# Kernel optimization log

Hardware: AMD Instinct MI355X
Metric: run time of the kernel (lower is better)

The kernel has to match this reference:

```python
import jax, jax.numpy as jnp
import numpy as np

B, C, RED, H, RANK = 32768, 1024, 4, 4, 16
CH = C // RED          # 256 hidden width after gated down-projection
DH = CH // H           # 64 head dim
RATIO = 0.5            # residual_ratio
LN_EPS = 1e-5


def setup_inputs() -> dict:
    key = jax.random.key(0)
    ks = iter(jax.random.split(key, 32))
    n = lambda shape, s=0.02: jax.random.normal(next(ks), shape, jnp.float32) * s
    return {
        "x": jax.random.normal(next(ks), (B, C), jnp.float32),
        # LayerNorm(c_in)
        "ln_g": jnp.ones((C,), jnp.float32),
        "ln_b": jnp.zeros((C,), jnp.float32),
        # gated linear: down_proj / gate_proj  (stored [in, out])
        "Wd": n((C, CH)), "bd": jnp.zeros((CH,), jnp.float32),
        "Wg": n((C, CH)), "bg": jnp.zeros((CH,), jnp.float32),
        # depthwise Conv1d(CH, CH, k=1, groups=CH) on length-1 seq -> per-channel affine
        "dw_w": n((CH,), 1.0), "dw_b": jnp.zeros((CH,), jnp.float32),
        # LightFNN: Linear-GELU-Linear
        "W1": n((CH, CH)), "b1": jnp.zeros((CH,), jnp.float32),
        "W2": n((CH, CH)), "b2": jnp.zeros((CH,), jnp.float32),
        # MHSA (seq_len = 1)
        "Wq": n((CH, CH)), "bq": jnp.zeros((CH,), jnp.float32),
        "Wk": n((CH, CH)), "bk": jnp.zeros((CH,), jnp.float32),
        "Wv": n((CH, CH)), "bv": jnp.zeros((CH,), jnp.float32),
        "Wo": n((CH, CH)), "bo": jnp.zeros((CH,), jnp.float32),
        # up_proj
        "Wu": n((CH, C)), "bu": jnp.zeros((C,), jnp.float32),
        # LoRA (bias-free)
        "Wld": n((C, RANK)), "Wlu": n((RANK, C)),
    }


def reference(x, ln_g, ln_b, Wd, bd, Wg, bg, dw_w, dw_b,
              W1, b1, W2, b2, Wq, bq, Wk, bk, Wv, bv, Wo, bo,
              Wu, bu, Wld, Wlu):
    residual = x
    # LayerNorm
    mu = jnp.mean(x, axis=-1, keepdims=True)
    var = jnp.mean(jnp.square(x - mu), axis=-1, keepdims=True)
    h = (x - mu) * jax.lax.rsqrt(var + LN_EPS) * ln_g + ln_b
    # gated linear unit
    h = (h @ Wd + bd) * jax.nn.sigmoid(h @ Wg + bg)          # [B, CH]
    # depthwise conv over length-1 sequence == per-channel affine
    h = h * dw_w + dw_b
    # light FFN
    h = jax.nn.gelu(h @ W1 + b1) @ W2 + b2
    # seq_len-1 self-attention: softmax over a single key is 1 => out = Wo(v)
    q = (h @ Wq + bq).reshape(B, H, DH)
    k = (h @ Wk + bk).reshape(B, H, DH)
    v = (h @ Wv + bv).reshape(B, H, DH)
    scores = jnp.sum(q * k, axis=-1, keepdims=True) / jnp.sqrt(jnp.float32(DH))  # [B,H,1]
    attn = jax.nn.softmax(scores, axis=-1)                   # == ones
    h = (attn * v).reshape(B, CH) @ Wo + bo
    # up projection + LoRA
    h = h @ Wu + bu                                          # [B, C]
    h = h + (h @ Wld) @ Wlu
    # dropout is identity at inference; weighted residual mix
    return RATIO * h + (1.0 - RATIO) * residual
```

## Files before the change

kernel.cpp:

```cpp
#include <hip/hip_runtime.h>
#include <hip/hip_bf16.h>
#include <stdint.h>


typedef float f32x4 __attribute__((ext_vector_type(4)));
typedef __bf16 bf16x8 __attribute__((ext_vector_type(8)));
typedef unsigned short u16x8 __attribute__((ext_vector_type(8)));
typedef unsigned short u16x4 __attribute__((ext_vector_type(4)));

#define LN_EPS 1e-5f

__device__ __forceinline__ unsigned short f2bf(float f) {
  unsigned int u = __float_as_uint(f);
  u += 0x7fffu + ((u >> 16) & 1u);
  return (unsigned short)(u >> 16);
}

__device__ __forceinline__ void bar_lds() {
  asm volatile("s_waitcnt lgkmcnt(0)\n\ts_barrier" ::: "memory");
}

__global__ __launch_bounds__(256) void k_prep(
    const float* __restrict__ ln_g, const float* __restrict__ ln_b,
    const float* __restrict__ Wd, const float* __restrict__ Wg,
    const float* __restrict__ dw_w, const float* __restrict__ dw_b,
    const float* __restrict__ W1, const float* __restrict__ b1,
    const float* __restrict__ W2, const float* __restrict__ b2,
    const float* __restrict__ Wv, const float* __restrict__ bv,
    const float* __restrict__ Wo, const float* __restrict__ bo,
    const float* __restrict__ Wu, const float* __restrict__ bu,
    const float* __restrict__ Wld, const float* __restrict__ Wlu,
    unsigned short* __restrict__ PGd, unsigned short* __restrict__ PGg,
    unsigned short* __restrict__ PW1, float* __restrict__ GP,
    float* __restrict__ b1p, float* __restrict__ X,
    float* __restrict__ Y, float* __restrict__ bcomb) {
  __shared__ alignas(16) char SMEM[32896];
  const int b = blockIdx.x, tid = threadIdx.x;

  if (b < 72) {
    float (*S)[257] = (float(*)[257])SMEM;
    const float* src; const float* scale; unsigned short* dst;
    int kc; int gpa = -1;
    if (b < 32)      { src = Wd; scale = ln_g; dst = PGd; kc = b;      gpa = 0; }
    else if (b < 64) { src = Wg; scale = ln_g; dst = PGg; kc = b - 32; gpa = 2; }
    else             { src = W1; scale = dw_w; dst = PW1; kc = b - 64; }
    float csg = 0.f, csb = 0.f;
    for (int r = 0; r < 32; ++r) {
      int k = kc * 32 + r;
      float raw = src[(size_t)k * 256 + tid];
      float v = scale[k] * raw;
      S[r][tid] = v;
      if (gpa >= 0) { csg += v; csb += ln_b[k] * raw; }
    }
    if (gpa >= 0) {
      GP[((size_t)gpa * 32 + kc) * 256 + tid] = csg;
      GP[((size_t)(gpa + 1) * 32 + kc) * 256 + tid] = csb;
    }
    __syncthreads();
    const int ntL = tid >> 4;
    #pragma unroll
    for (int c = 0; c < 4; ++c) {
      int lane = (tid * 4 + c) & 63;
      int kb = (lane >> 4) * 8, nl = ntL * 16 + (lane & 15);
      u16x8 o;
      #pragma unroll
      for (int j = 0; j < 8; ++j) o[j] = f2bf(S[kb + j][nl]);
      *(u16x8*)(dst + ((size_t)(kc * 16 + ntL) * 64 + lane) * 8) = o;
    }
  } else if (b == 72) {
    float s = 0.f;
    #pragma unroll 8
    for (int k = 0; k < 256; ++k) s += dw_b[k] * W1[k * 256 + tid];
    b1p[tid] = b1[tid] + s;
  } else if (b == 73) {
    float* F = (float*)SMEM;
    float* r1 = F;
    float* r2 = F + 256;
    float* r3 = F + 512;
    float* s16 = F + 1536;
    float* PART = F + 1552;
    float* sb = F + 1808;
    sb[tid] = b2[tid];
    __syncthreads();
    {
      float s = bv[tid];
      #pragma unroll 8
      for (int k = 0; k < 256; ++k) s += sb[k] * Wv[(size_t)k * 256 + tid];
      r1[tid] = s;
    }
    __syncthreads();
    {
      float s = bo[tid];
      #pragma unroll 8
      for (int k = 0; k < 256; ++k) s += r1[k] * Wo[(size_t)k * 256 + tid];
      r2[tid] = s;
    }
    __syncthreads();
    {
      float a0 = bu[tid], a1 = bu[tid + 256], a2 = bu[tid + 512], a3 = bu[tid + 768];
      #pragma unroll 4
      for (int k = 0; k < 256; ++k) {
        float rr = r2[k];
        const float* wr = Wu + (size_t)k * 1024 + tid;
        a0 += rr * wr[0]; a1 += rr * wr[256]; a2 += rr * wr[512]; a3 += rr * wr[768];
      }
      r3[tid] = a0; r3[tid + 256] = a1; r3[tid + 512] = a2; r3[tid + 768] = a3;
    }
    __syncthreads();
    {
      const int g = tid >> 4, s = tid & 15;
      float p = 0.f;
      #pragma unroll 4
      for (int n = g * 64; n < g * 64 + 64; ++n) p += r3[n] * Wld[(size_t)n * 16 + s];
      PART[g * 16 + s] = p;
    }
    __syncthreads();
    if (tid < 16) {
      float s = 0.f;
      #pragma unroll
      for (int g = 0; g < 16; ++g) s += PART[g * 16 + tid];
      s16[tid] = s;
    }
    __syncthreads();
    #pragma unroll
    for (int c = 0; c < 4; ++c) {
      int n = tid + c * 256;
      float v = r3[n];
      #pragma unroll
      for (int s = 0; s < 16; ++s) v += s16[s] * Wlu[(size_t)s * 1024 + n];
      bcomb[n] = v;
    }
  } else if (b < 90) {
    float (*SW)[257] = (float(*)[257])SMEM;
    const int r0 = (b - 74) * 16;
    #pragma unroll
    for (int r = 0; r < 16; ++r) SW[r][tid] = W2[(size_t)(r0 + r) * 256 + tid];
    __syncthreads();
    float acc[16];
    #pragma unroll
    for (int r = 0; r < 16; ++r) acc[r] = 0.f;
    #pragma unroll 4
    for (int n = 0; n < 256; ++n) {
      float wv = Wv[(size_t)n * 256 + tid];
      #pragma unroll
      for (int r = 0; r < 16; ++r) acc[r] += SW[r][n] * wv;
    }
    #pragma unroll
    for (int r = 0; r < 16; ++r) X[(size_t)(r0 + r) * 256 + tid] = acc[r];
  } else {
    float (*SW)[257] = (float(*)[257])SMEM;
    const int idx = b - 90, r0 = (idx >> 2) * 16, c0 = (idx & 3) * 256;
    #pragma unroll
    for (int r = 0; r < 16; ++r) SW[r][tid] = Wo[(size_t)(r0 + r) * 256 + tid];
    __syncthreads();
    float acc[16];
    #pragma unroll
    for (int r = 0; r < 16; ++r) acc[r] = 0.f;
    #pragma unroll 4
    for (int n = 0; n < 256; ++n) {
      float wu = Wu[(size_t)n * 1024 + c0 + tid];
      #pragma unroll
      for (int r = 0; r < 16; ++r) acc[r] += SW[r][n] * wu;
    }
    #pragma unroll
    for (int r = 0; r < 16; ++r) Y[(size_t)(r0 + r) * 1024 + c0 + tid] = acc[r];
  }
}

__global__ __launch_bounds__(256) void k_fold(
    const float* __restrict__ Y, const float* __restrict__ Wld,
    const float* __restrict__ Wlu, const float* __restrict__ GP,
    unsigned short* __restrict__ PY,
    float* __restrict__ gdvA, float* __restrict__ ggvA,
    float* __restrict__ bdA, float* __restrict__ bgA) {
  __shared__ alignas(16) char SMEM[32896];
  const int b = blockIdx.x, tid = threadIdx.x;
  if (b < 64) {
    float* F = (float*)SMEM;
    float* YLL = F;
    float* WL = F + 512;
    float* PART = F + 2560;
    unsigned short* TL = (unsigned short*)(SMEM + 10240);
    const int rb = b >> 3, ccol = (b & 7) * 128;
    {
      const int r = tid >> 3, g = tid & 7;
      const float* yrow = Y + (size_t)(rb * 32 + r) * 1024;
      float p[16];
      #pragma unroll
      for (int s = 0; s < 16; ++s) p[s] = 0.f;
      for (int n = g * 128; n < g * 128 + 128; ++n) {
        float yv = yrow[n];
        const float* wl = Wld + (size_t)n * 16;
        #pragma unroll
        for (int s = 0; s < 16; ++s) p[s] += yv * wl[s];
      }
      #pragma unroll
      for (int s = 0; s < 16; ++s) PART[(r * 16 + s) * 8 + g] = p[s];
    }
    __syncthreads();
    #pragma unroll
    for (int e2 = 0; e2 < 2; ++e2) {
      int e = tid + e2 * 256;
      float s = 0.f;
      #pragma unroll
      for (int g = 0; g < 8; ++g) s += PART[e * 8 + g];
      YLL[e] = s;
    }
    #pragma unroll
    for (int i = 0; i < 8; ++i) {
      int el = tid + i * 256;
      int s = el >> 7, n = el & 127;
      WL[el] = Wlu[(size_t)s * 1024 + ccol + n];
    }
    __syncthreads();
    const int r = tid >> 3, c0 = (tid & 7) * 16;
    const float* yrow = Y + (size_t)(rb * 32 + r) * 1024 + ccol + c0;
    float acc[16];
    #pragma unroll
    for (int cc = 0; cc < 4; ++cc) {
      f32x4 yv = *(const f32x4*)(yrow + cc * 4);
      #pragma unroll
      for (int j = 0; j < 4; ++j) acc[cc * 4 + j] = yv[j];
    }
    #pragma unroll
    for (int s = 0; s < 16; ++s) {
      float m = YLL[r * 16 + s];
      #pragma unroll
      for (int c = 0; c < 16; ++c) acc[c] += m * WL[s * 128 + c0 + c];
    }
    #pragma unroll
    for (int c = 0; c < 16; ++c) TL[r * 132 + c0 + c] = f2bf(acc[c]);
    __syncthreads();
    const int ntL = tid >> 5;
    #pragma unroll
    for (int hlf = 0; hlf < 2; ++hlf) {
      int lane = (tid & 31) + hlf * 32;
      int kb = (lane >> 4) * 8, nl = ntL * 16 + (lane & 15);
      u16x8 o;
      #pragma unroll
      for (int j = 0; j < 8; ++j) o[j] = TL[(kb + j) * 132 + nl];
      *(u16x8*)(PY + ((size_t)(rb * 64 + (b & 7) * 8 + ntL) * 64 + lane) * 8) = o;
    }
  } else {
    float s0 = 0.f, s1 = 0.f, s2 = 0.f, s3 = 0.f;
    for (int kc2 = 0; kc2 < 32; ++kc2) {
      s0 += GP[((size_t)0 * 32 + kc2) * 256 + tid];
      s1 += GP[((size_t)1 * 32 + kc2) * 256 + tid];
      s2 += GP[((size_t)2 * 32 + kc2) * 256 + tid];
      s3 += GP[((size_t)3 * 32 + kc2) * 256 + tid];
    }
    gdvA[tid] = s0; bdA[tid] = s1; ggvA[tid] = s2; bgA[tid] = s3;
  }
}

__global__ __launch_bounds__(256) void k_wcomb(
    const float* __restrict__ X, const unsigned short* __restrict__ PY,
    unsigned short* __restrict__ PWc) {
  __shared__ alignas(16) char SMEM[32896];
  unsigned short* XA2 = (unsigned short*)SMEM;
  unsigned short* TL = XA2 + 2048;
  const int b = blockIdx.x, tid = threadIdx.x;
  const int rb = b >> 4, cg = b & 15;
  const int w = tid >> 6, l = tid & 63, q = l >> 4, m15 = l & 15;
  const int r0 = rb * 32;
  const int srow = tid >> 3;
  const int kk = (tid & 7) * 4;
  const int rt = srow >> 4, m = srow & 15;
  const int xaidx = rt * 512 + ((kk >> 3) * 16 + m) * 8 + (kk & 7);
  const float* arow = X + (size_t)(r0 + srow) * 256 + kk;
  f32x4 acc0 = {0.f, 0.f, 0.f, 0.f}, acc1 = {0.f, 0.f, 0.f, 0.f};
  float4 v = *(const float4*)arow;
  for (int kc = 0; kc < 8; ++kc) {
    unsigned short* xp = XA2 + (kc & 1) * 1024;
    u16x4 hv; hv[0] = f2bf(v.x); hv[1] = f2bf(v.y); hv[2] = f2bf(v.z); hv[3] = f2bf(v.w);
    *(u16x4*)&xp[xaidx] = hv;
    if (kc < 7) v = *(const float4*)(arow + (kc + 1) * 32);
    bar_lds();
    bf16x8 bf = *(const bf16x8*)(PY + ((size_t)(kc * 64 + cg * 4 + w) * 64 + l) * 8);
    bf16x8 af0 = *(const bf16x8*)&xp[l * 8];
    bf16x8 af1 = *(const bf16x8*)&xp[512 + l * 8];
    acc0 = __builtin_amdgcn_mfma_f32_16x16x32_bf16(af0, bf, acc0, 0, 0, 0);
    acc1 = __builtin_amdgcn_mfma_f32_16x16x32_bf16(af1, bf, acc1, 0, 0, 0);
  }
  #pragma unroll
  for (int r = 0; r < 4; ++r) {
    TL[(q * 4 + r) * 68 + w * 16 + m15] = f2bf(acc0[r]);
    TL[(16 + q * 4 + r) * 68 + w * 16 + m15] = f2bf(acc1[r]);
  }
  bar_lds();
  const int ntL = tid >> 6, lane = tid & 63;
  const int kb = (lane >> 4) * 8, nl = ntL * 16 + (lane & 15);
  u16x8 o;
  #pragma unroll
  for (int j = 0; j < 8; ++j) o[j] = TL[(kb + j) * 68 + nl];
  *(u16x8*)(PWc + ((size_t)(rb * 64 + cg * 4 + ntL) * 64 + lane) * 8) = o;
}

__global__ __launch_bounds__(512, 4) void k_main(
    const float* __restrict__ x,
    const unsigned short* __restrict__ PGd, const unsigned short* __restrict__ PGg,
    const unsigned short* __restrict__ PW1, const unsigned short* __restrict__ PWc,
    const float* __restrict__ gdvA, const float* __restrict__ ggvA,
    const float* __restrict__ bdA, const float* __restrict__ bgA,
    const float* __restrict__ bd, const float* __restrict__ bg,
    const float* __restrict__ b1p, const float* __restrict__ bcomb,
    float* __restrict__ out) {
  __shared__ unsigned short XA[2][2048];
  __shared__ unsigned short HBUF[16384];
  __shared__ float SMS[1024];
  __shared__ float MURS[128];
  __shared__ float OBUF[16 * 260];

  const int tid = threadIdx.x;
  const int w = tid >> 6, l = tid & 63, q = l >> 4, m15 = l & 15;
  const int row0 = blockIdx.x * 64;

  float gdc[2], ggc[2], bdc[2], bgc[2], b1c[2];
  #pragma unroll
  for (int i = 0; i < 2; ++i) {
    int col = w * 32 + i * 16 + m15;
    gdc[i] = gdvA[col]; ggc[i] = ggvA[col];
    bdc[i] = bdA[col] + bd[col];
    bgc[i] = bgA[col] + bg[col];
    b1c[i] = b1p[col];
  }

  f32x4 accd[4][2], accg[4][2];
  const f32x4 zero4 = {0.f, 0.f, 0.f, 0.f};
  #pragma unroll
  for (int mt = 0; mt < 4; ++mt)
    #pragma unroll
    for (int i = 0; i < 2; ++i) { accd[mt][i] = zero4; accg[mt][i] = zero4; }

  const int srow = tid >> 3, sseg = tid & 7;
  const float* xrow = x + (size_t)(row0 + srow) * 1024 + sseg * 4;
  const int xaidx = (((srow >> 4) * 64 + (sseg >> 1) * 16 + (srow & 15)) << 3) + (sseg & 1) * 4;
  float ssum = 0.f, ssq = 0.f;

  float4 v = *(const float4*)xrow;
  for (int kc = 0; kc < 32; ++kc) {
    const int p = kc & 1;
    u16x4 hv; hv[0] = f2bf(v.x); hv[1] = f2bf(v.y); hv[2] = f2bf(v.z); hv[3] = f2bf(v.w);
    *(u16x4*)&XA[p][xaidx] = hv;
    ssum += v.x + v.y + v.z + v.w;
    ssq += v.x * v.x + v.y * v.y + v.z * v.z + v.w * v.w;
    if (kc < 31) v = *(const float4*)(xrow + (kc + 1) * 32);
    bar_lds();
    bf16x8 fd[2], fg[2];
    #pragma unroll
    for (int i = 0; i < 2; ++i) {
      size_t off = ((size_t)(kc * 16 + w * 2 + i) * 64 + l) * 8;
      fd[i] = *(const bf16x8*)(PGd + off);
      fg[i] = *(const bf16x8*)(PGg + off);
    }
    #pragma unroll
    for (int mt = 0; mt < 4; ++mt) {
      bf16x8 af = *(const bf16x8*)&XA[p][(mt * 64 + l) * 8];
      #pragma unroll
      for (int i = 0; i < 2; ++i) {
        accd[mt][i] = __builtin_amdgcn_mfma_f32_16x16x32_bf16(af, fd[i], accd[mt][i], 0, 0, 0);
        accg[mt][i] = __builtin_amdgcn_mfma_f32_16x16x32_bf16(af, fg[i], accg[mt][i], 0, 0, 0);
      }
    }
  }

  SMS[tid] = ssum;
  SMS[512 + tid] = ssq;
  bar_lds();
  if (tid < 64) {
    float s = 0.f, sq = 0.f;
    #pragma unroll
    for (int p2 = 0; p2 < 8; ++p2) { s += SMS[tid * 8 + p2]; sq += SMS[512 + tid * 8 + p2]; }
    float mu = s * (1.f / 1024.f);
    float var = sq * (1.f / 1024.f) - mu * mu;
    MURS[tid * 2] = mu;
    MURS[tid * 2 + 1] = rsqrtf(var + LN_EPS);
  }
  bar_lds();

  #pragma unroll
  for (int i = 0; i < 2; ++i) {
    int q2 = i * 2 + (m15 >> 3), j2 = m15 & 7;
    #pragma unroll
    for (int mt = 0; mt < 4; ++mt) {
      #pragma unroll
      for (int r = 0; r < 4; ++r) {
        int row = mt * 16 + q * 4 + r;
        float mu = MURS[row * 2], rs = MURS[row * 2 + 1];
        float pd = rs * (accd[mt][i][r] - mu * gdc[i]) + bdc[i];
        float pg = rs * (accg[mt][i][r] - mu * ggc[i]) + bgc[i];
        float hv = pd / (1.f + __expf(-pg));
        HBUF[((mt * 8 + w) * 64 + q2 * 16 + q * 4 + r) * 8 + j2] = f2bf(hv);
      }
    }
  }
  bar_lds();

  f32x4 acc2[4][2];
  #pragma unroll
  for (int mt = 0; mt < 4; ++mt)
    #pragma unroll
    for (int i = 0; i < 2; ++i) acc2[mt][i] = zero4;
  for (int kc = 0; kc < 8; ++kc) {
    bf16x8 bf[2];
    #pragma unroll
    for (int i = 0; i < 2; ++i)
      bf[i] = *(const bf16x8*)(PW1 + ((size_t)(kc * 16 + w * 2 + i) * 64 + l) * 8);
    #pragma unroll
    for (int mt = 0; mt < 4; ++mt) {
      bf16x8 af = *(const bf16x8*)&HBUF[((mt * 8 + kc) * 64 + l) * 8];
      #pragma unroll
      for (int i = 0; i < 2; ++i)
        acc2[mt][i] = __builtin_amdgcn_mfma_f32_16x16x32_bf16(af, bf[i], acc2[mt][i], 0, 0, 0);
    }
  }
  bar_lds();
  #pragma unroll
  for (int i = 0; i < 2; ++i) {
    int q2 = i * 2 + (m15 >> 3), j2 = m15 & 7;
    #pragma unroll
    for (int mt = 0; mt < 4; ++mt) {
      #pragma unroll
      for (int r = 0; r < 4; ++r) {
        float vv = acc2[mt][i][r] + b1c[i];
        float u = 0.7978845608f * (vv + 0.044715f * vv * vv * vv);
        float th = 1.f - 2.f / (1.f + __expf(2.f * u));
        HBUF[((mt * 8 + w) * 64 + q2 * 16 + q * 4 + r) * 8 + j2] = f2bf(0.5f * vv * (1.f + th));
      }
    }
  }
  bar_lds();

  for (int nc = 0; nc < 4; ++nc) {
    f32x4 acc3[4][2];
    #pragma unroll
    for (int mt = 0; mt < 4; ++mt)
      #pragma unroll
      for (int i = 0; i < 2; ++i) acc3[mt][i] = zero4;
    for (int kc = 0; kc < 8; ++kc) {
      bf16x8 bf[2];
      #pragma unroll
      for (int i = 0; i < 2; ++i)
        bf[i] = *(const bf16x8*)(PWc + ((size_t)(kc * 64 + nc * 16 + w * 2 + i) * 64 + l) * 8);
      #pragma unroll
      for (int mt = 0; mt < 4; ++mt) {
        bf16x8 af = *(const bf16x8*)&HBUF[((mt * 8 + kc) * 64 + l) * 8];
        #pragma unroll
        for (int i = 0; i < 2; ++i)
          acc3[mt][i] = __builtin_amdgcn_mfma_f32_16x16x32_bf16(af, bf[i], acc3[mt][i], 0, 0, 0);
      }
    }
    float bc[2];
    #pragma unroll
    for (int i = 0; i < 2; ++i) bc[i] = bcomb[nc * 256 + w * 32 + i * 16 + m15];
    const int rowL = tid >> 5, c0 = (tid & 31) * 4;
    #pragma unroll
    for (int mt = 0; mt < 4; ++mt) {
      #pragma unroll
      for (int r = 0; r < 4; ++r)
        #pragma unroll
        for (int i = 0; i < 2; ++i)
          OBUF[(q * 4 + r) * 260 + w * 32 + i * 16 + m15] = acc3[mt][i][r] + bc[i];
      bar_lds();
      const size_t gbase = (size_t)(row0 + mt * 16 + rowL) * 1024 + nc * 256;
      #pragma unroll
      for (int h = 0; h < 2; ++h) {
        int cc = c0 + h * 128;
        f32x4 yv = *(const f32x4*)&OBUF[rowL * 260 + cc];
        float4 xr = *(const float4*)(x + gbase + cc);
        float4 o;
        o.x = 0.5f * yv[0] + 0.5f * xr.x;
        o.y = 0.5f * yv[1] + 0.5f * xr.y;
        o.z = 0.5f * yv[2] + 0.5f * xr.z;
        o.w = 0.5f * yv[3] + 0.5f * xr.w;
        *(float4*)(out + gbase + cc) = o;
      }
      bar_lds();
    }
  }
}

extern "C" void kernel_launch(void* const* d_in, const int* in_sizes, int n_in,
                              void* d_out, int out_size, void* d_ws, size_t ws_size,
                              hipStream_t stream) {
  (void)in_sizes; (void)n_in; (void)out_size; (void)ws_size;
  const float* x    = (const float*)d_in[0];
  const float* ln_g = (const float*)d_in[1];
  const float* ln_b = (const float*)d_in[2];
  const float* Wd   = (const float*)d_in[3];
  const float* bd   = (const float*)d_in[4];
  const float* Wg   = (const float*)d_in[5];
  const float* bg   = (const float*)d_in[6];
  const float* dw_w = (const float*)d_in[7];
  const float* dw_b = (const float*)d_in[8];
  const float* W1   = (const float*)d_in[9];
  const float* b1   = (const float*)d_in[10];
  const float* W2   = (const float*)d_in[11];
  const float* b2   = (const float*)d_in[12];
  const float* Wv   = (const float*)d_in[17];
  const float* bv   = (const float*)d_in[18];
  const float* Wo   = (const float*)d_in[19];
  const float* bo   = (const float*)d_in[20];
  const float* Wu   = (const float*)d_in[21];
  const float* bu   = (const float*)d_in[22];
  const float* Wld  = (const float*)d_in[23];
  const float* Wlu  = (const float*)d_in[24];
  float* out = (float*)d_out;

  char* ws = (char*)d_ws;
  unsigned short* PGd = (unsigned short*)(ws + 0);
  unsigned short* PGg = (unsigned short*)(ws + 524288);
  unsigned short* PW1 = (unsigned short*)(ws + 1048576);
  unsigned short* PY  = (unsigned short*)(ws + 1310720);
  unsigned short* PWc = (unsigned short*)(ws + 1835008);
  float* X     = (float*)(ws + 2359296);
  float* Y     = (float*)(ws + 2621440);
  float* GP    = (float*)(ws + 3670016);
  float* gdvA  = (float*)(ws + 3801088);
  float* ggvA  = (float*)(ws + 3802112);
  float* bdA   = (float*)(ws + 3803136);
  float* bgA   = (float*)(ws + 3804160);
  float* b1p   = (float*)(ws + 3805184);
  float* bcomb = (float*)(ws + 3806208);

  hipLaunchKernelGGL(k_prep, dim3(154), dim3(256), 0, stream,
                     ln_g, ln_b, Wd, Wg, dw_w, dw_b, W1, b1, W2, b2,
                     Wv, bv, Wo, bo, Wu, bu, Wld, Wlu,
                     PGd, PGg, PW1, GP, b1p, X, Y, bcomb);
  hipLaunchKernelGGL(k_fold, dim3(65), dim3(256), 0, stream,
                     Y, Wld, Wlu, GP, PY, gdvA, ggvA, bdA, bgA);
  hipLaunchKernelGGL(k_wcomb, dim3(128), dim3(256), 0, stream, X, PY, PWc);
  hipLaunchKernelGGL(k_main, dim3(512), dim3(512), 0, stream,
                     x, PGd, PGg, PW1, PWc, gdvA, ggvA, bdA, bgA, bd, bg, b1p, bcomb, out);
}
```

Measured before the change: 457.4 us.

## Merge weight-fold kernels into prep and wcomb, parallelize bias chain

The weight-preprocessing pipeline shrinks from four launches to three. The Wo·Wu product and its LoRA fold now run in the prep kernel, which writes the packed PY operand directly, and k_fold is removed. The serial single-block bias chain (b2→Wv→Wo→Wu→LoRA) is split into parallel blocks, with the final combine reassociated into the wcomb kernel. This cuts a launch and the serial critical path, at the cost of heavier per-block work in prep and different floating-point summation order.

```diff
diff --git a/kernel.cpp b/kernel.cpp
--- a/kernel.cpp
+++ b/kernel.cpp
@@ -24,7 +24,7 @@
     const float* __restrict__ ln_g, const float* __restrict__ ln_b,
     const float* __restrict__ Wd, const float* __restrict__ Wg,
     const float* __restrict__ dw_w, const float* __restrict__ dw_b,
-    const float* __restrict__ W1, const float* __restrict__ b1,
+    const float* __restrict__ W1,
     const float* __restrict__ W2, const float* __restrict__ b2,
     const float* __restrict__ Wv, const float* __restrict__ bv,
     const float* __restrict__ Wo, const float* __restrict__ bo,
@@ -32,9 +32,10 @@
     const float* __restrict__ Wld, const float* __restrict__ Wlu,
     unsigned short* __restrict__ PGd, unsigned short* __restrict__ PGg,
     unsigned short* __restrict__ PW1, float* __restrict__ GP,
-    float* __restrict__ b1p, float* __restrict__ X,
-    float* __restrict__ Y, float* __restrict__ bcomb) {
-  __shared__ alignas(16) char SMEM[32896];
+    float* __restrict__ GPB, float* __restrict__ r1,
+    float* __restrict__ t0, float* __restrict__ X,
+    unsigned short* __restrict__ PY, float* __restrict__ Y3) {
+  __shared__ alignas(16) char SMEM[49664];
   const int b = blockIdx.x, tid = threadIdx.x;
 
   if (b < 72) {
@@ -67,51 +68,176 @@
       for (int j = 0; j < 8; ++j) o[j] = f2bf(S[kb + j][nl]);
       *(u16x8*)(dst + ((size_t)(kc * 16 + ntL) * 64 + lane) * 8) = o;
     }
-  } else if (b == 72) {
+  } else if (b < 80) {
+    const int kc = b - 72;
     float s = 0.f;
+    #pragma unroll
+    for (int k = 0; k < 32; ++k)
+      s += dw_b[kc * 32 + k] * W1[(size_t)(kc * 32 + k) * 256 + tid];
+    GPB[(size_t)kc * 256 + tid] = s;
+  } else if (b == 80) {
+    float s = bv[tid];
     #pragma unroll 8
-    for (int k = 0; k < 256; ++k) s += dw_b[k] * W1[k * 256 + tid];
-    b1p[tid] = b1[tid] + s;
-  } else if (b == 73) {
+    for (int k = 0; k < 256; ++k) s += b2[k] * Wv[(size_t)k * 256 + tid];
+    r1[tid] = s;
+  } else if (b < 85) {
+    const int c0 = (b - 81) * 256;
+    float s = bu[c0 + tid];
+    #pragma unroll 8
+    for (int k = 0; k < 256; ++k) s += bo[k] * Wu[(size_t)k * 1024 + c0 + tid];
+    t0[c0 + tid] = s;
+  } else if (b < 101) {
+    const int r0 = (b - 85) * 16;
+    float acc[16];
+    #pragma unroll
+    for (int r = 0; r < 16; ++r) acc[r] = 0.f;
+    #pragma unroll 4
+    for (int n = 0; n < 256; ++n) {
+      float wv = Wv[(size_t)n * 256 + tid];
+      #pragma unroll
+      for (int r = 0; r < 16; ++r) acc[r] += W2[(size_t)(r0 + r) * 256 + n] * wv;
+    }
+    #pragma unroll
+    for (int r = 0; r < 16; ++r) X[(size_t)(r0 + r) * 256 + tid] = acc[r];
+  } else {
+    float* YS = (float*)SMEM;
+    float* PART = (float*)(SMEM + 32768);
+    float* YL = (float*)(SMEM + 49152);
+    const int rb = b - 101;
+    const int r0 = rb * 8;
+    const int c0 = tid * 4;
+    f32x4 acc[8];
+    #pragma unroll
+    for (int r = 0; r < 8; ++r) acc[r] = (f32x4){0.f, 0.f, 0.f, 0.f};
+    #pragma unroll 4
+    for (int k = 0; k < 256; ++k) {
+      f32x4 wu = *(const f32x4*)(Wu + (size_t)k * 1024 + c0);
+      #pragma unroll
+      for (int r = 0; r < 8; ++r) {
+        float wo = Wo[(size_t)(r0 + r) * 256 + k];
+        #pragma unroll
+        for (int j = 0; j < 4; ++j) acc[r][j] += wo * wu[j];
+      }
+    }
+    #pragma unroll
+    for (int r = 0; r < 8; ++r) *(f32x4*)&YS[r * 1024 + c0] = acc[r];
+    __syncthreads();
+    {
+      const int r = tid >> 5, g = tid & 31;
+      float p[16];
+      #pragma unroll
+      for (int s = 0; s < 16; ++s) p[s] = 0.f;
+      for (int i = 0; i < 32; ++i) {
+        int n = g + i * 32;
+        float yv = YS[r * 1024 + n];
+        const float* wl = Wld + (size_t)n * 16;
+        #pragma unroll
+        for (int s = 0; s < 16; ++s) p[s] += yv * wl[s];
+      }
+      #pragma unroll
+      for (int s = 0; s < 16; ++s) PART[(r * 16 + s) * 32 + g] = p[s];
+    }
+    __syncthreads();
+    if (tid < 128) {
+      float s = 0.f;
+      #pragma unroll
+      for (int g = 0; g < 32; ++g) s += PART[tid * 32 + g];
+      YL[tid] = s;
+    }
+    __syncthreads();
+    f32x4 y3[8];
+    #pragma unroll
+    for (int r = 0; r < 8; ++r) y3[r] = *(const f32x4*)&YS[r * 1024 + c0];
+    #pragma unroll
+    for (int s = 0; s < 16; ++s) {
+      f32x4 wl = *(const f32x4*)(Wlu + (size_t)s * 1024 + c0);
+      #pragma unroll
+      for (int r = 0; r < 8; ++r) {
+        float m = YL[r * 16 + s];
+        #pragma unroll
+        for (int j = 0; j < 4; ++j) y3[r][j] += m * wl[j];
+      }
+    }
+    #pragma unroll
+    for (int r = 0; r < 8; ++r)
+      *(f32x4*)(Y3 + (size_t)(r0 + r) * 1024 + c0) = y3[r];
+    const int kc = rb >> 2, a = rb & 3;
+    #pragma unroll
+    for (int j2 = 0; j2 < 4; ++j2) {
+      int c = c0 + j2;
+      int nt = c >> 4, lane = a * 16 + (c & 15);
+      u16x8 o;
+      #pragma unroll
+      for (int j = 0; j < 8; ++j) o[j] = f2bf(y3[j][j2]);
+      *(u16x8*)(PY + ((size_t)(kc * 64 + nt) * 64 + lane) * 8) = o;
+    }
+  }
+}
+
+__global__ __launch_bounds__(256) void k_wcomb(
+    const float* __restrict__ X, const unsigned short* __restrict__ PY,
+    unsigned short* __restrict__ PWc,
+    const float* __restrict__ r1, const float* __restrict__ t0,
+    const float* __restrict__ Wld, const float* __restrict__ Wlu,
+    const float* __restrict__ Y3, const float* __restrict__ GP,
+    const float* __restrict__ GPB, const float* __restrict__ b1,
+    float* __restrict__ gdvA, float* __restrict__ ggvA,
+    float* __restrict__ bdA, float* __restrict__ bgA,
+    float* __restrict__ b1p, float* __restrict__ bcomb) {
+  __shared__ alignas(16) char SMEM[32896];
+  const int b = blockIdx.x, tid = threadIdx.x;
+  if (b < 128) {
+    unsigned short* XA2 = (unsigned short*)SMEM;
+    unsigned short* TL = XA2 + 2048;
+    const int rb = b >> 4, cg = b & 15;
+    const int w = tid >> 6, l = tid & 63, q = l >> 4, m15 = l & 15;
+    const int r0 = rb * 32;
+    const int srow = tid >> 3;
+    const int kk = (tid & 7) * 4;
+    const int rt = srow >> 4, m = srow & 15;
+    const int xaidx = rt * 512 + ((kk >> 3) * 16 + m) * 8 + (kk & 7);
+    const float* arow = X + (size_t)(r0 + srow) * 256 + kk;
+    f32x4 acc0 = {0.f, 0.f, 0.f, 0.f}, acc1 = {0.f, 0.f, 0.f, 0.f};
+    float4 v = *(const float4*)arow;
+    for (int kc = 0; kc < 8; ++kc) {
+      unsigned short* xp = XA2 + (kc & 1) * 1024;
+      u16x4 hv; hv[0] = f2bf(v.x); hv[1] = f2bf(v.y); hv[2] = f2bf(v.z); hv[3] = f2bf(v.w);
+      *(u16x4*)&xp[xaidx] = hv;
+      if (kc < 7) v = *(const float4*)(arow + (kc + 1) * 32);
+      bar_lds();
+      bf16x8 bf = *(const bf16x8*)(PY + ((size_t)(kc * 64 + cg * 4 + w) * 64 + l) * 8);
+      bf16x8 af0 = *(const bf16x8*)&xp[l * 8];
+      bf16x8 af1 = *(const bf16x8*)&xp[512 + l * 8];
+      acc0 = __builtin_amdgcn_mfma_f32_16x16x32_bf16(af0, bf, acc0, 0, 0, 0);
+      acc1 = __builtin_amdgcn_mfma_f32_16x16x32_bf16(af1, bf, acc1, 0, 0, 0);
+    }
+    #pragma unroll
+    for (int r = 0; r < 4; ++r) {
+      TL[(q * 4 + r) * 68 + w * 16 + m15] = f2bf(acc0[r]);
+      TL[(16 + q * 4 + r) * 68 + w * 16 + m15] = f2bf(acc1[r]);
+    }
+    bar_lds();
+    const int ntL = tid >> 6, lane = tid & 63;
+    const int kb = (lane >> 4) * 8, nl = ntL * 16 + (lane & 15);
+    u16x8 o;
+    #pragma unroll
+    for (int j = 0; j < 8; ++j) o[j] = TL[(kb + j) * 68 + nl];
+    *(u16x8*)(PWc + ((size_t)(rb * 64 + cg * 4 + ntL) * 64 + lane) * 8) = o;
+  } else if (b == 128) {
     float* F = (float*)SMEM;
-    float* r1 = F;
-    float* r2 = F + 256;
-    float* r3 = F + 512;
-    float* s16 = F + 1536;
-    float* PART = F + 1552;
-    float* sb = F + 1808;
-    sb[tid] = b2[tid];
-    __syncthreads();
-    {
-      float s = bv[tid];
-      #pragma unroll 8
-      for (int k = 0; k < 256; ++k) s += sb[k] * Wv[(size_t)k * 256 + tid];
-      r1[tid] = s;
-    }
-    __syncthreads();
-    {
-      float s = bo[tid];
-      #pragma unroll 8
-      for (int k = 0; k < 256; ++k) s += r1[k] * Wo[(size_t)k * 256 + tid];
-      r2[tid] = s;
-    }
-    __syncthreads();
-    {
-      float a0 = bu[tid], a1 = bu[tid + 256], a2 = bu[tid + 512], a3 = bu[tid + 768];
-      #pragma unroll 4
-      for (int k = 0; k < 256; ++k) {
-        float rr = r2[k];
-        const float* wr = Wu + (size_t)k * 1024 + tid;
-        a0 += rr * wr[0]; a1 += rr * wr[256]; a2 += rr * wr[512]; a3 += rr * wr[768];
-      }
-      r3[tid] = a0; r3[tid + 256] = a1; r3[tid + 512] = a2; r3[tid + 768] = a3;
-    }
+    float* R1 = F;
+    float* T0 = F + 256;
+    float* PART = F + 1280;
+    float* U16 = F + 1536;
+    R1[tid] = r1[tid];
+    #pragma unroll
+    for (int c2 = 0; c2 < 4; ++c2) T0[tid + c2 * 256] = t0[tid + c2 * 256];
     __syncthreads();
     {
       const int g = tid >> 4, s = tid & 15;
       float p = 0.f;
       #pragma unroll 4
-      for (int n = g * 64; n < g * 64 + 64; ++n) p += r3[n] * Wld[(size_t)n * 16 + s];
+      for (int n = g * 64; n < g * 64 + 64; ++n) p += T0[n] * Wld[(size_t)n * 16 + s];
       PART[g * 16 + s] = p;
     }
     __syncthreads();
@@ -119,128 +245,28 @@
       float s = 0.f;
       #pragma unroll
       for (int g = 0; g < 16; ++g) s += PART[g * 16 + tid];
-      s16[tid] = s;
-    }
-    __syncthreads();
-    #pragma unroll
-    for (int c = 0; c < 4; ++c) {
-      int n = tid + c * 256;
-      float v = r3[n];
-      #pragma unroll
-      for (int s = 0; s < 16; ++s) v += s16[s] * Wlu[(size_t)s * 1024 + n];
-      bcomb[n] = v;
-    }
-  } else if (b < 90) {
-    float (*SW)[257] = (float(*)[257])SMEM;
-    const int r0 = (b - 74) * 16;
-    #pragma unroll
-    for (int r = 0; r < 16; ++r) SW[r][tid] = W2[(size_t)(r0 + r) * 256 + tid];
-    __syncthreads();
-    float acc[16];
-    #pragma unroll
-    for (int r = 0; r < 16; ++r) acc[r] = 0.f;
+      U16[tid] = s;
+    }
+    __syncthreads();
+    const int c0 = tid * 4;
+    f32x4 rv = {0.f, 0.f, 0.f, 0.f};
     #pragma unroll 4
-    for (int n = 0; n < 256; ++n) {
-      float wv = Wv[(size_t)n * 256 + tid];
-      #pragma unroll
-      for (int r = 0; r < 16; ++r) acc[r] += SW[r][n] * wv;
-    }
-    #pragma unroll
-    for (int r = 0; r < 16; ++r) X[(size_t)(r0 + r) * 256 + tid] = acc[r];
-  } else {
-    float (*SW)[257] = (float(*)[257])SMEM;
-    const int idx = b - 90, r0 = (idx >> 2) * 16, c0 = (idx & 3) * 256;
-    #pragma unroll
-    for (int r = 0; r < 16; ++r) SW[r][tid] = Wo[(size_t)(r0 + r) * 256 + tid];
-    __syncthreads();
-    float acc[16];
-    #pragma unroll
-    for (int r = 0; r < 16; ++r) acc[r] = 0.f;
-    #pragma unroll 4
-    for (int n = 0; n < 256; ++n) {
-      float wu = Wu[(size_t)n * 1024 + c0 + tid];
-      #pragma unroll
-      for (int r = 0; r < 16; ++r) acc[r] += SW[r][n] * wu;
-    }
-    #pragma unroll
-    for (int r = 0; r < 16; ++r) Y[(size_t)(r0 + r) * 1024 + c0 + tid] = acc[r];
-  }
-}
-
-__global__ __launch_bounds__(256) void k_fold(
-    const float* __restrict__ Y, const float* __restrict__ Wld,
-    const float* __restrict__ Wlu, const float* __restrict__ GP,
-    unsigned short* __restrict__ PY,
-    float* __restrict__ gdvA, float* __restrict__ ggvA,
-    float* __restrict__ bdA, float* __restrict__ bgA) {
-  __shared__ alignas(16) char SMEM[32896];
-  const int b = blockIdx.x, tid = threadIdx.x;
-  if (b < 64) {
-    float* F = (float*)SMEM;
-    float* YLL = F;
-    float* WL = F + 512;
-    float* PART = F + 2560;
-    unsigned short* TL = (unsigned short*)(SMEM + 10240);
-    const int rb = b >> 3, ccol = (b & 7) * 128;
-    {
-      const int r = tid >> 3, g = tid & 7;
-      const float* yrow = Y + (size_t)(rb * 32 + r) * 1024;
-      float p[16];
-      #pragma unroll
-      for (int s = 0; s < 16; ++s) p[s] = 0.f;
-      for (int n = g * 128; n < g * 128 + 128; ++n) {
-        float yv = yrow[n];
-        const float* wl = Wld + (size_t)n * 16;
-        #pragma unroll
-        for (int s = 0; s < 16; ++s) p[s] += yv * wl[s];
-      }
-      #pragma unroll
-      for (int s = 0; s < 16; ++s) PART[(r * 16 + s) * 8 + g] = p[s];
-    }
-    __syncthreads();
-    #pragma unroll
-    for (int e2 = 0; e2 < 2; ++e2) {
-      int e = tid + e2 * 256;
-      float s = 0.f;
-      #pragma unroll
-      for (int g = 0; g < 8; ++g) s += PART[e * 8 + g];
-      YLL[e] = s;
-    }
-    #pragma unroll
-    for (int i = 0; i < 8; ++i) {
-      int el = tid + i * 256;
-      int s = el >> 7, n = el & 127;
-      WL[el] = Wlu[(size_t)s * 1024 + ccol + n];
-    }
-    __syncthreads();
-    const int r = tid >> 3, c0 = (tid & 7) * 16;
-    const float* yrow = Y + (size_t)(rb * 32 + r) * 1024 + ccol + c0;
-    float acc[16];
-    #pragma unroll
-    for (int cc = 0; cc < 4; ++cc) {
-      f32x4 yv = *(const f32x4*)(yrow + cc * 4);
-      #pragma unroll
-      for (int j = 0; j < 4; ++j) acc[cc * 4 + j] = yv[j];
-    }
+    for (int k = 0; k < 256; ++k) {
+      f32x4 yv = *(const f32x4*)(Y3 + (size_t)k * 1024 + c0);
+      float rk = R1[k];
+      #pragma unroll
+      for (int j = 0; j < 4; ++j) rv[j] += rk * yv[j];
+    }
+    f32x4 vv;
+    #pragma unroll
+    for (int j = 0; j < 4; ++j) vv[j] = T0[c0 + j] + rv[j];
     #pragma unroll
     for (int s = 0; s < 16; ++s) {
-      float m = YLL[r * 16 + s];
-      #pragma unroll
-      for (int c = 0; c < 16; ++c) acc[c] += m * WL[s * 128 + c0 + c];
-    }
-    #pragma unroll
-    for (int c = 0; c < 16; ++c) TL[r * 132 + c0 + c] = f2bf(acc[c]);
-    __syncthreads();
-    const int ntL = tid >> 5;
-    #pragma unroll
-    for (int hlf = 0; hlf < 2; ++hlf) {
-      int lane = (tid & 31) + hlf * 32;
-      int kb = (lane >> 4) * 8, nl = ntL * 16 + (lane & 15);
-      u16x8 o;
-      #pragma unroll
-      for (int j = 0; j < 8; ++j) o[j] = TL[(kb + j) * 132 + nl];
-      *(u16x8*)(PY + ((size_t)(rb * 64 + (b & 7) * 8 + ntL) * 64 + lane) * 8) = o;
-    }
+      f32x4 wl = *(const f32x4*)(Wlu + (size_t)s * 1024 + c0);
+      #pragma unroll
+      for (int j = 0; j < 4; ++j) vv[j] += U16[s] * wl[j];
+    }
+    *(f32x4*)(bcomb + c0) = vv;
   } else {
     float s0 = 0.f, s1 = 0.f, s2 = 0.f, s3 = 0.f;
     for (int kc2 = 0; kc2 < 32; ++kc2) {
@@ -250,50 +276,11 @@
       s3 += GP[((size_t)3 * 32 + kc2) * 256 + tid];
     }
     gdvA[tid] = s0; bdA[tid] = s1; ggvA[tid] = s2; bgA[tid] = s3;
-  }
-}
-
-__global__ __launch_bounds__(256) void k_wcomb(
-    const float* __restrict__ X, const unsigned short* __restrict__ PY,
-    unsigned short* __restrict__ PWc) {
-  __shared__ alignas(16) char SMEM[32896];
-  unsigned short* XA2 = (unsigned short*)SMEM;
-  unsigned short* TL = XA2 + 2048;
-  const int b = blockIdx.x, tid = threadIdx.x;
-  const int rb = b >> 4, cg = b & 15;
-  const int w = tid >> 6, l = tid & 63, q = l >> 4, m15 = l & 15;
-  const int r0 = rb * 32;
-  const int srow = tid >> 3;
-  const int kk = (tid & 7) * 4;
-  const int rt = srow >> 4, m = srow & 15;
-  const int xaidx = rt * 512 + ((kk >> 3) * 16 + m) * 8 + (kk & 7);
-  const float* arow = X + (size_t)(r0 + srow) * 256 + kk;
-  f32x4 acc0 = {0.f, 0.f, 0.f, 0.f}, acc1 = {0.f, 0.f, 0.f, 0.f};
-  float4 v = *(const float4*)arow;
-  for (int kc = 0; kc < 8; ++kc) {
-    unsigned short* xp = XA2 + (kc & 1) * 1024;
-    u16x4 hv; hv[0] = f2bf(v.x); hv[1] = f2bf(v.y); hv[2] = f2bf(v.z); hv[3] = f2bf(v.w);
-    *(u16x4*)&xp[xaidx] = hv;
-    if (kc < 7) v = *(const float4*)(arow + (kc + 1) * 32);
-    bar_lds();
-    bf16x8 bf = *(const bf16x8*)(PY + ((size_t)(kc * 64 + cg * 4 + w) * 64 + l) * 8);
-    bf16x8 af0 = *(const bf16x8*)&xp[l * 8];
-    bf16x8 af1 = *(const bf16x8*)&xp[512 + l * 8];
-    acc0 = __builtin_amdgcn_mfma_f32_16x16x32_bf16(af0, bf, acc0, 0, 0, 0);
-    acc1 = __builtin_amdgcn_mfma_f32_16x16x32_bf16(af1, bf, acc1, 0, 0, 0);
-  }
-  #pragma unroll
-  for (int r = 0; r < 4; ++r) {
-    TL[(q * 4 + r) * 68 + w * 16 + m15] = f2bf(acc0[r]);
-    TL[(16 + q * 4 + r) * 68 + w * 16 + m15] = f2bf(acc1[r]);
-  }
-  bar_lds();
-  const int ntL = tid >> 6, lane = tid & 63;
-  const int kb = (lane >> 4) * 8, nl = ntL * 16 + (lane & 15);
-  u16x8 o;
-  #pragma unroll
-  for (int j = 0; j < 8; ++j) o[j] = TL[(kb + j) * 68 + nl];
-  *(u16x8*)(PWc + ((size_t)(rb * 64 + cg * 4 + ntL) * 64 + lane) * 8) = o;
+    float sb1 = b1[tid];
+    #pragma unroll
+    for (int p = 0; p < 8; ++p) sb1 += GPB[(size_t)p * 256 + tid];
+    b1p[tid] = sb1;
+  }
 }
 
 __global__ __launch_bounds__(512, 4) void k_main(
@@ -514,7 +501,7 @@
   unsigned short* PY  = (unsigned short*)(ws + 1310720);
   unsigned short* PWc = (unsigned short*)(ws + 1835008);
   float* X     = (float*)(ws + 2359296);
-  float* Y     = (float*)(ws + 2621440);
+  float* Y3    = (float*)(ws + 2621440);
   float* GP    = (float*)(ws + 3670016);
   float* gdvA  = (float*)(ws + 3801088);
   float* ggvA  = (float*)(ws + 3802112);
@@ -522,14 +509,17 @@
   float* bgA   = (float*)(ws + 3804160);
   float* b1p   = (float*)(ws + 3805184);
   float* bcomb = (float*)(ws + 3806208);
-
-  hipLaunchKernelGGL(k_prep, dim3(154), dim3(256), 0, stream,
-                     ln_g, ln_b, Wd, Wg, dw_w, dw_b, W1, b1, W2, b2,
+  float* r1    = (float*)(ws + 3810304);
+  float* t0    = (float*)(ws + 3811328);
+  float* GPB   = (float*)(ws + 3815424);
+
+  hipLaunchKernelGGL(k_prep, dim3(133), dim3(256), 0, stream,
+                     ln_g, ln_b, Wd, Wg, dw_w, dw_b, W1, W2, b2,
                      Wv, bv, Wo, bo, Wu, bu, Wld, Wlu,
-                     PGd, PGg, PW1, GP, b1p, X, Y, bcomb);
-  hipLaunchKernelGGL(k_fold, dim3(65), dim3(256), 0, stream,
-                     Y, Wld, Wlu, GP, PY, gdvA, ggvA, bdA, bgA);
-  hipLaunchKernelGGL(k_wcomb, dim3(128), dim3(256), 0, stream, X, PY, PWc);
+                     PGd, PGg, PW1, GP, GPB, r1, t0, X, PY, Y3);
+  hipLaunchKernelGGL(k_wcomb, dim3(130), dim3(256), 0, stream,
+                     X, PY, PWc, r1, t0, Wld, Wlu, Y3, GP, GPB, b1,
+                     gdvA, ggvA, bdA, bgA, b1p, bcomb);
   hipLaunchKernelGGL(k_main, dim3(512), dim3(512), 0, stream,
                      x, PGd, PGg, PW1, PWc, gdvA, ggvA, bdA, bgA, bd, bg, b1p, bcomb, out);
 }
```

Measured after the change: 404.2 us. 1.13x faster.
